# Performance work log

Hardware: AMD Instinct MI355X
Metric: run time of the kernel (lower is better)

The kernel has to match this reference:

```python
import jax, jax.numpy as jnp
import numpy as np

B = 4096  # number of rows (batch of 1-D sequences)
N = 4096  # transform length


def setup_inputs() -> dict:
    key = jax.random.key(0)
    x = jax.random.normal(key, (B, N), dtype=jnp.float32)
    # get_expk(N): expk[k] = (cos(pi*k/(2N)), -sin(pi*k/(2N)))
    t = jnp.arange(N, dtype=jnp.float32) * (np.pi / (2.0 * N))
    expk = jnp.stack([jnp.cos(t), -jnp.sin(t)], axis=-1)  # [N, 2]
    return {"x": x, "expk": expk}


def reference(x, expk):
    # IDCT (DCT-III), 2N-point FFT formulation:
    #   y_k = x_0 + 2 * sum_{n=1}^{N-1} x_n cos(pi*n*(2k+1)/(2N))
    #       = Re{ sum_n w_n x_n exp(j*pi*n/(2N)) * exp(j*2*pi*n*k/(2N)) },  w_0=1, w_n=2
    # i.e. the first N outputs of a 2N-point inverse DFT of the zero-padded,
    # twiddle-premultiplied sequence.
    n = x.shape[-1]
    # expk stores (cos(theta), -sin(theta)) => exp(+j*theta) = expk0 - j*expk1
    coef = (expk[..., 0] - 1j * expk[..., 1]).astype(jnp.complex64)  # [N]
    w = jnp.concatenate([jnp.ones((1,), x.dtype), jnp.full((n - 1,), 2.0, x.dtype)])
    a = (x * w).astype(jnp.complex64) * coef                      # [B, N]
    A = jnp.concatenate([a, jnp.zeros_like(a)], axis=-1)          # [B, 2N] zero-pad
    y = jnp.real(jnp.fft.ifft(A, axis=-1))[..., :n] * (2.0 * n)   # undo 1/(2N) of ifft
    return y.astype(x.dtype)
```

## Files before the change

### kernel.cpp

```cpp
#include <hip/hip_runtime.h>


#define NROW 4096
#define MM   2048
#define NT   256
#define SWZ(a) ((a) ^ ((((a) >> 6) & 7) << 1))

__device__ __forceinline__ void cmul(float ar, float ai, float br, float bi,
                                     float& orr, float& oii) {
    orr = ar * br - ai * bi;
    oii = ar * bi + ai * br;
}

__device__ __forceinline__ void dft4(float& ar, float& ai, float& br, float& bi,
                                     float& cr, float& ci, float& dr, float& di) {
    float s02r = ar + cr, s02i = ai + ci;
    float d02r = ar - cr, d02i = ai - ci;
    float s13r = br + dr, s13i = bi + di;
    float d13r = br - dr, d13i = bi - di;
    ar = s02r + s13r; ai = s02i + s13i;
    br = d02r - d13i; bi = d02i + d13r;
    cr = s02r - s13r; ci = s02i - s13i;
    dr = d02r + d13i; di = d02i - d13r;
}

__device__ __forceinline__ void dft8(float* vr, float* vi) {
    float er[4]  = {vr[0], vr[2], vr[4], vr[6]};
    float ei[4]  = {vi[0], vi[2], vi[4], vi[6]};
    float odr[4] = {vr[1], vr[3], vr[5], vr[7]};
    float odi[4] = {vi[1], vi[3], vi[5], vi[7]};
    dft4(er[0], ei[0], er[1], ei[1], er[2], ei[2], er[3], ei[3]);
    dft4(odr[0], odi[0], odr[1], odi[1], odr[2], odi[2], odr[3], odi[3]);
    const float s = 0.70710678118654752f;
    vr[0] = er[0] + odr[0];            vi[0] = ei[0] + odi[0];
    vr[4] = er[0] - odr[0];            vi[4] = ei[0] - odi[0];
    float t1r = s * (odr[1] - odi[1]), t1i = s * (odr[1] + odi[1]);
    vr[1] = er[1] + t1r;               vi[1] = ei[1] + t1i;
    vr[5] = er[1] - t1r;               vi[5] = ei[1] - t1i;
    vr[2] = er[2] - odi[2];            vi[2] = ei[2] + odr[2];
    vr[6] = er[2] + odi[2];            vi[6] = ei[2] - odr[2];
    float t3r = -s * (odr[3] + odi[3]), t3i = s * (odr[3] - odi[3]);
    vr[3] = er[3] + t3r;               vi[3] = ei[3] + t3i;
    vr[7] = er[3] - t3r;               vi[7] = ei[3] - t3i;
}

__device__ __forceinline__ void twiddle_in8(float* vr, float* vi,
                                            float w1r, float w1i) {
    float cr = w1r, ci = w1i;
#pragma unroll
    for (int r = 1; r < 8; ++r) {
        float tr, ti;
        cmul(vr[r], vi[r], cr, ci, tr, ti);
        vr[r] = tr; vi[r] = ti;
        if (r < 7) { float nr, ni; cmul(cr, ci, w1r, w1i, nr, ni); cr = nr; ci = ni; }
    }
}

extern "C" __global__ void __launch_bounds__(NT, 6)
idct_fft_kernel(const float* __restrict__ x, const float* __restrict__ expk,
                float* __restrict__ out)
{
    __shared__ __align__(16) float2 BA[MM];
    __shared__ __align__(16) float2 BB[MM];
    const int tid = threadIdx.x;
    const long row = blockIdx.x;
    const float* __restrict__ xp = x + row * (long)NROW;
    const float2* __restrict__ e2 = (const float2*)expk;

    float vr[8], vi[8];

#pragma unroll
    for (int r = 0; r < 8; ++r) {
        int k = tid + NT * r;
        float x1  = xp[k];
        float x2  = xp[k + MM];
        float xr1 = (k == 0) ? 0.0f : xp[NROW - k];
        float xr2 = xp[MM - k];
        float2 E1 = e2[k];
        float2 E2 = e2[k + MM];
        float c1 = E1.x, s1 = -E1.y;
        float c2 = E2.x, s2 = -E2.y;
        float h1r = c1 * x1 + s1 * xr1, h1i = s1 * x1 - c1 * xr1;
        float h2r = c2 * x2 + s2 * xr2, h2i = s2 * x2 - c2 * xr2;
        int hi = (k >= 1024);
        float2 EW = e2[(4 * k) & (NROW - 1)];
        float wr = hi ? EW.y : EW.x;
        float wi = hi ? EW.x : -EW.y;
        float Sr = h1r + h2r, Si = h1i + h2i;
        float Dr = h1r - h2r, Di = h1i - h2i;
        vr[r] = Sr - (wr * Di + wi * Dr);
        vi[r] = Si + (wr * Dr - wi * Di);
    }
    dft8(vr, vi);
#pragma unroll
    for (int j = 0; j < 4; ++j) {
        int a = 8 * tid + 2 * j;
        *(float4*)&BA[SWZ(a)] =
            make_float4(vr[2 * j], vi[2 * j], vr[2 * j + 1], vi[2 * j + 1]);
    }
    __syncthreads();

#pragma unroll
    for (int r = 0; r < 8; ++r) {
        float2 c = BA[SWZ(tid + 256 * r)];
        vr[r] = c.x; vi[r] = c.y;
    }
    {
        float2 E = e2[256 * (tid & 7)];
        twiddle_in8(vr, vi, E.x, -E.y);
    }
    dft8(vr, vi);
    {
        int p = tid & 7, t = tid >> 3;
#pragma unroll
        for (int q = 0; q < 8; ++q)
            BB[SWZ(p + 8 * q + 64 * t)] = make_float2(vr[q], vi[q]);
    }
    __syncthreads();

#pragma unroll
    for (int r = 0; r < 8; ++r) {
        float2 c = BB[SWZ(tid + 256 * r)];
        vr[r] = c.x; vi[r] = c.y;
    }
    {
        float2 E = e2[32 * (tid & 63)];
        twiddle_in8(vr, vi, E.x, -E.y);
    }
    dft8(vr, vi);
    {
        int p = tid & 63, t = tid >> 6;
#pragma unroll
        for (int q = 0; q < 8; ++q)
            BA[SWZ(p + 64 * q + 512 * t)] = make_float2(vr[q], vi[q]);
    }
    __syncthreads();

    float ar[4], ai[4], br4[4], bi4[4];
    const int pB = 511 - tid;
#pragma unroll
    for (int r = 0; r < 4; ++r) {
        float2 cA = BA[SWZ(tid + 512 * r)];
        ar[r] = cA.x; ai[r] = cA.y;
        float2 cB = BA[SWZ(pB + 512 * r)];
        br4[r] = cB.x; bi4[r] = cB.y;
    }
    {
        float2 EA = e2[8 * tid];
        float wAr = EA.x, wAi = -EA.y, cr = wAr, ci = wAi;
#pragma unroll
        for (int r = 1; r < 4; ++r) {
            float tr, ti; cmul(ar[r], ai[r], cr, ci, tr, ti); ar[r] = tr; ai[r] = ti;
            if (r < 3) { float nr, ni; cmul(cr, ci, wAr, wAi, nr, ni); cr = nr; ci = ni; }
        }
        float2 EB = e2[8 * pB];
        float wBr = EB.x, wBi = -EB.y; cr = wBr; ci = wBi;
#pragma unroll
        for (int r = 1; r < 4; ++r) {
            float tr, ti; cmul(br4[r], bi4[r], cr, ci, tr, ti); br4[r] = tr; bi4[r] = ti;
            if (r < 3) { float nr, ni; cmul(cr, ci, wBr, wBi, nr, ni); cr = nr; ci = ni; }
        }
    }
    dft4(ar[0], ai[0], ar[1], ai[1], ar[2], ai[2], ar[3], ai[3]);
    dft4(br4[0], bi4[0], br4[1], bi4[1], br4[2], bi4[2], br4[3], bi4[3]);

    float4* __restrict__ y4 = (float4*)(out + row * (long)NROW);
    y4[tid]        = make_float4(ar[0],  bi4[3], ai[0],  br4[3]);
    y4[tid + 512]  = make_float4(ar[1],  bi4[2], ai[1],  br4[2]);
    y4[1023 - tid] = make_float4(br4[1], ai[2],  bi4[1], ar[2]);
    y4[511 - tid]  = make_float4(br4[0], ai[3],  bi4[0], ar[3]);
}

extern "C" void kernel_launch(void* const* d_in, const int* in_sizes, int n_in,
                              void* d_out, int out_size, void* d_ws, size_t ws_size,
                              hipStream_t stream) {
    const float* x    = (const float*)d_in[0];
    const float* expk = (const float*)d_in[1];
    float* out        = (float*)d_out;
    const int nrows   = in_sizes[0] / NROW;
    hipLaunchKernelGGL(idct_fft_kernel, dim3(nrows), dim3(NT), 0, stream,
                       x, expk, out);
}
```

Measured before the change: 133.6 us.

## Use single shared buffer with extra barriers and compute twiddles from expk

Merges the two 16KB shared-memory ping-pong buffers into one 16KB buffer, adding barriers after each read phase so it can be safely overwritten, and raises the launch-bounds occupancy hint from 6 to 8 blocks per CU. It also replaces the expk loads for the second-half and 4k twiddles with arithmetic derived from the first twiddle via angle-addition and double-angle identities. This cuts LDS footprint and global/cache traffic to allow more resident blocks, at the cost of two extra barriers, more ALU work, and slightly different floating-point rounding of the twiddles.

```diff
diff --git a/kernel.cpp b/kernel.cpp
--- a/kernel.cpp
+++ b/kernel.cpp
@@ -56,12 +56,11 @@
     }
 }
 
-extern "C" __global__ void __launch_bounds__(NT, 6)
+extern "C" __global__ void __launch_bounds__(NT, 8)
 idct_fft_kernel(const float* __restrict__ x, const float* __restrict__ expk,
                 float* __restrict__ out)
 {
-    __shared__ __align__(16) float2 BA[MM];
-    __shared__ __align__(16) float2 BB[MM];
+    __shared__ __align__(16) float2 S[MM];
     const int tid = threadIdx.x;
     const long row = blockIdx.x;
     const float* __restrict__ xp = x + row * (long)NROW;
@@ -69,6 +68,7 @@
 
     float vr[8], vi[8];
 
+    const float R2H = 0.70710678118654752f;
 #pragma unroll
     for (int r = 0; r < 8; ++r) {
         int k = tid + NT * r;
@@ -77,15 +77,15 @@
         float xr1 = (k == 0) ? 0.0f : xp[NROW - k];
         float xr2 = xp[MM - k];
         float2 E1 = e2[k];
-        float2 E2 = e2[k + MM];
         float c1 = E1.x, s1 = -E1.y;
-        float c2 = E2.x, s2 = -E2.y;
+        float c2 = (c1 - s1) * R2H;
+        float s2 = (c1 + s1) * R2H;
+        float c2t = 2.0f * c1 * c1 - 1.0f;
+        float s2t = 2.0f * s1 * c1;
+        float wr  = 2.0f * c2t * c2t - 1.0f;
+        float wi  = 2.0f * s2t * c2t;
         float h1r = c1 * x1 + s1 * xr1, h1i = s1 * x1 - c1 * xr1;
         float h2r = c2 * x2 + s2 * xr2, h2i = s2 * x2 - c2 * xr2;
-        int hi = (k >= 1024);
-        float2 EW = e2[(4 * k) & (NROW - 1)];
-        float wr = hi ? EW.y : EW.x;
-        float wi = hi ? EW.x : -EW.y;
         float Sr = h1r + h2r, Si = h1i + h2i;
         float Dr = h1r - h2r, Di = h1i - h2i;
         vr[r] = Sr - (wr * Di + wi * Dr);
@@ -95,16 +95,17 @@
 #pragma unroll
     for (int j = 0; j < 4; ++j) {
         int a = 8 * tid + 2 * j;
-        *(float4*)&BA[SWZ(a)] =
+        *(float4*)&S[SWZ(a)] =
             make_float4(vr[2 * j], vi[2 * j], vr[2 * j + 1], vi[2 * j + 1]);
     }
     __syncthreads();
 
 #pragma unroll
     for (int r = 0; r < 8; ++r) {
-        float2 c = BA[SWZ(tid + 256 * r)];
+        float2 c = S[SWZ(tid + 256 * r)];
         vr[r] = c.x; vi[r] = c.y;
     }
+    __syncthreads();
     {
         float2 E = e2[256 * (tid & 7)];
         twiddle_in8(vr, vi, E.x, -E.y);
@@ -114,15 +115,16 @@
         int p = tid & 7, t = tid >> 3;
 #pragma unroll
         for (int q = 0; q < 8; ++q)
-            BB[SWZ(p + 8 * q + 64 * t)] = make_float2(vr[q], vi[q]);
+            S[SWZ(p + 8 * q + 64 * t)] = make_float2(vr[q], vi[q]);
     }
     __syncthreads();
 
 #pragma unroll
     for (int r = 0; r < 8; ++r) {
-        float2 c = BB[SWZ(tid + 256 * r)];
+        float2 c = S[SWZ(tid + 256 * r)];
         vr[r] = c.x; vi[r] = c.y;
     }
+    __syncthreads();
     {
         float2 E = e2[32 * (tid & 63)];
         twiddle_in8(vr, vi, E.x, -E.y);
@@ -132,7 +134,7 @@
         int p = tid & 63, t = tid >> 6;
 #pragma unroll
         for (int q = 0; q < 8; ++q)
-            BA[SWZ(p + 64 * q + 512 * t)] = make_float2(vr[q], vi[q]);
+            S[SWZ(p + 64 * q + 512 * t)] = make_float2(vr[q], vi[q]);
     }
     __syncthreads();
 
@@ -140,9 +142,9 @@
     const int pB = 511 - tid;
 #pragma unroll
     for (int r = 0; r < 4; ++r) {
-        float2 cA = BA[SWZ(tid + 512 * r)];
+        float2 cA = S[SWZ(tid + 512 * r)];
         ar[r] = cA.x; ai[r] = cA.y;
-        float2 cB = BA[SWZ(pB + 512 * r)];
+        float2 cB = S[SWZ(pB + 512 * r)];
         br4[r] = cB.x; bi4[r] = cB.y;
     }
     {
```

Result: faster. 124.9 us (-6.5%).
